# Performance work log

Measured on AMD Instinct MI355X. Metric: run time of the kernel, lower is better.

## Reference

```python
import jax, jax.numpy as jnp
import numpy as np

D = 1024
H = 16
N = 4096
D_K = D // H
SCALE = D_K ** 0.5


def setup_inputs() -> dict:
    key = jax.random.key(0)
    k_x, k_w = jax.random.split(key)
    X = jax.random.normal(k_x, (N, D), dtype=jnp.float32)
    # nn.Linear(D, 2*D, bias=False): weight [2D, D], y = X @ W.T
    Wqkv = jax.random.normal(k_w, (2 * D, D), dtype=jnp.float32) * (1.0 / np.sqrt(D))
    return {"X": X, "Wqkv": Wqkv}


def reference(X, Wqkv):
    n = X.shape[0]
    proj = X @ Wqkv.T                      # [N, 2D]
    qk, v = jnp.split(proj, 2, axis=-1)    # each [N, D]
    qk = qk.reshape(n, H, D_K)             # [N, H, d_k]
    v = v.reshape(n, H, D_K)
    s = jnp.einsum('nhd,mhd->hnm', qk, qk) / SCALE  # [H, N, N]
    a = jax.nn.softmax(s, axis=-1)
    ctx = jnp.einsum('hnm,mhd->nhd', a, v).reshape(n, H * D_K)
    return ctx
```

## Files before the change

kernel.cpp:

```cpp
#include <hip/hip_runtime.h>
#include <hip/hip_bf16.h>

#define N_TOK   4096
#define D_MODEL 1024
#define H_HEADS 16
#define DK      64
#define KVB     64
#define QK_PRESCALE 0.42466092f


typedef float  f32x4   __attribute__((ext_vector_type(4)));
typedef float  f32x16  __attribute__((ext_vector_type(16)));
typedef short  bf16x8  __attribute__((ext_vector_type(8)));

__device__ __forceinline__ ushort f2bf(float f) {
  union { float f; unsigned u; } v; v.f = f;
  unsigned u = v.u;
  u += 0x7fffu + ((u >> 16) & 1u);
  return (ushort)(u >> 16);
}

__device__ __forceinline__ unsigned cvt_pk_bf16(float lo, float hi) {
  unsigned r;
  asm("v_cvt_pk_bf16_f32 %0, %1, %2" : "=v"(r) : "v"(lo), "v"(hi));
  return r;
}

__device__ __forceinline__ float exp2_raw(float x) {
  float r;
  asm("v_exp_f32 %0, %1" : "=v"(r) : "v"(x));
  return r;
}

__device__ __forceinline__ void gload_lds16(const void* gsrc, void* ldst) {
  __builtin_amdgcn_global_load_lds(
      (const __attribute__((address_space(1))) unsigned int*)gsrc,
      (__attribute__((address_space(3))) unsigned int*)ldst, 16, 0, 0);
}

__device__ __forceinline__ f32x16 mfma32(bf16x8 a, bf16x8 b, f32x16 c) {
  return __builtin_amdgcn_mfma_f32_32x32x16_bf16(a, b, c, 0, 0, 0);
}

__device__ __forceinline__ void swap32(unsigned &a, unsigned &b) {
  asm("v_permlane32_swap_b32 %0, %1" : "+v"(a), "+v"(b));
}

__global__ __launch_bounds__(256) void cvt_bf16_kernel(
    const float* __restrict__ X, const float* __restrict__ W,
    ushort* __restrict__ Xb, ushort* __restrict__ Wb) {
  const size_t i = (size_t)blockIdx.x * 256 + threadIdx.x;
  const float* s;
  ushort* d;
  size_t off;
  if (i < 524288) { s = X; d = Xb; off = i * 8; }
  else            { s = W; d = Wb; off = (i - 524288) * 8; }
  float4 a = *(const float4*)(s + off);
  float4 b = *(const float4*)(s + off + 4);
  ushort4 lo, hi;
  lo.x = f2bf(a.x); lo.y = f2bf(a.y); lo.z = f2bf(a.z); lo.w = f2bf(a.w);
  hi.x = f2bf(b.x); hi.y = f2bf(b.y); hi.z = f2bf(b.z); hi.w = f2bf(b.w);
  *(ushort4*)(d + off)     = lo;
  *(ushort4*)(d + off + 4) = hi;
}

__global__ __launch_bounds__(256) void qkv_gemm_kernel(
    const ushort* __restrict__ Xb, const ushort* __restrict__ Wb,
    ushort* __restrict__ Qb, ushort* __restrict__ Vt) {
  __shared__ ushort As[2][128][32];
  __shared__ ushort Bs[2][128][32];

  const int tid  = threadIdx.x;
  const int lane = tid & 63;
  const int g    = lane >> 4;
  const int lr   = lane & 15;
  const int wave = tid >> 6;
  const int wr   = (wave >> 1) * 64;
  const int wc   = (wave & 1) * 64;

  const int bid = blockIdx.x;
  const int x   = bid & 7;
  const int i   = bid >> 3;
  const int rb  = (x >> 1) * 8 + (i >> 3);
  const int cb  = (x & 1) * 8 + (i & 7);

  f32x4 acc[4][4] = {};

  const int r0 = tid >> 2;
  const int c0 = (tid & 3) * 8;
  const ushort* xsrc = Xb + (size_t)(rb * 128 + r0) * D_MODEL + c0;
  const ushort* wsrc = Wb + (size_t)(cb * 128 + r0) * D_MODEL + c0;

#define GST(BUF, K0)                                                         \
  {                                                                          \
    gload_lds16(xsrc + (K0), (ushort*)As[BUF] + tid * 8);                    \
    gload_lds16(xsrc + 64 * D_MODEL + (K0), (ushort*)As[BUF] + (tid + 256) * 8); \
    gload_lds16(wsrc + (K0), (ushort*)Bs[BUF] + tid * 8);                    \
    gload_lds16(wsrc + 64 * D_MODEL + (K0), (ushort*)Bs[BUF] + (tid + 256) * 8); \
  }

  GST(0, 0);
  __syncthreads();

  for (int k0 = 0; k0 < D_MODEL; k0 += 32) {
    const int buf = (k0 >> 5) & 1;
    if (k0 + 32 < D_MODEL) GST(buf ^ 1, k0 + 32);

    bf16x8 a[4], b[4];
#pragma unroll
    for (int m = 0; m < 4; ++m) a[m] = *(const bf16x8*)&As[buf][wr + m * 16 + lr][g * 8];
#pragma unroll
    for (int n = 0; n < 4; ++n) b[n] = *(const bf16x8*)&Bs[buf][wc + n * 16 + lr][g * 8];

#pragma unroll
    for (int m = 0; m < 4; ++m)
#pragma unroll
      for (int n = 0; n < 4; ++n)
        acc[m][n] = __builtin_amdgcn_mfma_f32_16x16x32_bf16(a[m], b[n], acc[m][n], 0, 0, 0);
    __syncthreads();
  }

  const int nrow0 = rb * 128 + wr;
  const int jcol0 = cb * 128 + wc;
  if (cb < 8) {
#pragma unroll
    for (int m = 0; m < 4; ++m) {
      const int nn = nrow0 + m * 16 + 4 * g;
#pragma unroll
      for (int n = 0; n < 4; ++n) {
        const int j = jcol0 + n * 16 + lr;
#pragma unroll
        for (int r = 0; r < 4; ++r)
          Qb[(size_t)(nn + r) * D_MODEL + j] = f2bf(acc[m][n][r] * QK_PRESCALE);
      }
    }
  } else {
#pragma unroll
    for (int m = 0; m < 4; ++m) {
      const int nn = nrow0 + m * 16 + 4 * g;
#pragma unroll
      for (int n = 0; n < 4; ++n) {
        const int c = jcol0 - D_MODEL + n * 16 + lr;
        uint2 pv = { cvt_pk_bf16(acc[m][n][0], acc[m][n][1]),
                     cvt_pk_bf16(acc[m][n][2], acc[m][n][3]) };
        *(uint2*)(Vt + (size_t)c * N_TOK + nn) = pv;
      }
    }
  }
}

__global__ __launch_bounds__(512, 4) void attn_kernel(
    const ushort* __restrict__ Qb, const ushort* __restrict__ Vg,
    float* __restrict__ Out) {
  __shared__ __align__(16) char smem[65536];

  const int tid  = threadIdx.x;
  const int lane = tid & 63;
  const int l31  = lane & 31;
  const int hi   = lane >> 5;
  const int wave = tid >> 6;
  const int quad = wave >> 2;
  const int wq   = wave & 3;
  const int qtid = tid & 255;

  const int bid = blockIdx.x;
  const int i   = bid >> 3;
  const int h   = (bid & 7) * 2 + (i >> 5);
  const int qbase = (i & 31) * 128 + wq * 32;
  const int kvlo  = quad * (N_TOK / 2);
  const int nit   = (N_TOK / 2) / KVB;

  ushort* KtP = (ushort*)(smem + quad * 32768);
  ushort* VtP = (ushort*)(smem + quad * 32768 + 16384);

  bf16x8 qf[4];
  const ushort* qrow = Qb + (size_t)(qbase + l31) * D_MODEL + h * DK;
#pragma unroll
  for (int ks = 0; ks < 4; ++ks)
    qf[ks] = *(const bf16x8*)(qrow + ks * 16 + hi * 8);

  float l_run = 0.f;
  const f32x16 zz = {};
  f32x16 ctx0 = {}, ctx1 = {};

  const int srow = qtid >> 3;
  const int scg  = (qtid & 7) ^ (srow & 7);
  const ushort* kst = Qb + (size_t)(kvlo + srow) * D_MODEL + h * DK + scg * 8;
  const ushort* vst = Vg + (size_t)(h * DK + srow) * N_TOK + kvlo + scg * 8;

#define STAGE_ADV(BUF)                                                        \
  {                                                                           \
    ushort* kd = KtP + (BUF) * 4096 + (size_t)qtid * 8;                       \
    ushort* vd = VtP + (BUF) * 4096 + (size_t)qtid * 8;                       \
    gload_lds16(kst, kd);                                                     \
    gload_lds16(kst + 32 * D_MODEL, kd + 2048);                               \
    gload_lds16(vst, vd);                                                     \
    gload_lds16(vst + 32 * N_TOK, vd + 2048);                                 \
    kst += (size_t)KVB * D_MODEL;                                             \
    vst += KVB;                                                               \
  }

#define ATTN_BODY(BUF)                                                        \
  {                                                                           \
    if (stages_left > 0) { STAGE_ADV(BUF ^ 1); --stages_left; }               \
    f32x16 st0 = zz, st1 = zz;                                                \
    __builtin_amdgcn_s_setprio(1);                                            \
    _Pragma("unroll")                                                         \
    for (int ks = 0; ks < 4; ++ks) {                                          \
      bf16x8 kf0 = *(const bf16x8*)(KtP + (BUF) * 4096 + l31 * 64 +           \
                                    (((((ks << 1) | hi)) ^ (l31 & 7)) << 3)); \
      bf16x8 kf1 = *(const bf16x8*)(KtP + (BUF) * 4096 + (32 + l31) * 64 +    \
                                    (((((ks << 1) | hi)) ^ (l31 & 7)) << 3)); \
      st0 = mfma32(kf0, qf[ks], st0);                                         \
      st1 = mfma32(kf1, qf[ks], st1);                                         \
    }                                                                         \
    __builtin_amdgcn_s_setprio(0);                                            \
    float rsb[4];                                                             \
    unsigned pk0[8], pk1[8];                                                  \
    _Pragma("unroll")                                                         \
    for (int b = 0; b < 4; ++b) {                                             \
      float a0 = exp2_raw(st0[4 * b + 0]);                                    \
      float a1 = exp2_raw(st0[4 * b + 1]);                                    \
      float a2 = exp2_raw(st0[4 * b + 2]);                                    \
      float a3 = exp2_raw(st0[4 * b + 3]);                                    \
      float c0 = exp2_raw(st1[4 * b + 0]);                                    \
      float c1 = exp2_raw(st1[4 * b + 1]);                                    \
      float c2 = exp2_raw(st1[4 * b + 2]);                                    \
      float c3 = exp2_raw(st1[4 * b + 3]);                                    \
      rsb[b] = ((a0 + a1) + (a2 + a3)) + ((c0 + c1) + (c2 + c3));             \
      pk0[2 * b]     = cvt_pk_bf16(a0, a1);                                   \
      pk0[2 * b + 1] = cvt_pk_bf16(a2, a3);                                   \
      pk1[2 * b]     = cvt_pk_bf16(c0, c1);                                   \
      pk1[2 * b + 1] = cvt_pk_bf16(c2, c3);                                   \
    }                                                                         \
    l_run += (rsb[0] + rsb[1]) + (rsb[2] + rsb[3]);                           \
    _Pragma("unroll")                                                         \
    for (int kt = 0; kt < 2; ++kt) {                                          \
      _Pragma("unroll")                                                       \
      for (int km = 0; km < 2; ++km) {                                        \
        unsigned u0 = kt ? pk1[4 * km + 0] : pk0[4 * km + 0];                 \
        unsigned u1 = kt ? pk1[4 * km + 1] : pk0[4 * km + 1];                 \
        unsigned u2 = kt ? pk1[4 * km + 2] : pk0[4 * km + 2];                 \
        unsigned u3 = kt ? pk1[4 * km + 3] : pk0[4 * km + 3];                 \
        swap32(u0, u2);                                                       \
        swap32(u1, u3);                                                       \
        union { unsigned u[4]; bf16x8 v; } pf;                                \
        pf.u[0] = u0; pf.u[1] = u1; pf.u[2] = u2; pf.u[3] = u3;               \
        const int ck = (kt << 2) | (km << 1) | hi;                            \
        bf16x8 vf0 = *(const bf16x8*)(VtP + (BUF) * 4096 + l31 * 64 +         \
                                      ((ck ^ (l31 & 7)) << 3));               \
        bf16x8 vf1 = *(const bf16x8*)(VtP + (BUF) * 4096 + (32 + l31) * 64 +  \
                                      ((ck ^ (l31 & 7)) << 3));               \
        __builtin_amdgcn_s_setprio(1);                                        \
        ctx0 = mfma32(vf0, pf.v, ctx0);                                       \
        ctx1 = mfma32(vf1, pf.v, ctx1);                                       \
        __builtin_amdgcn_s_setprio(0);                                        \
      }                                                                       \
    }                                                                         \
    __syncthreads();                                                          \
  }

  int stages_left = nit - 1;
  STAGE_ADV(0);
  __syncthreads();

  for (int it = 0; it < nit; it += 2) {
    ATTN_BODY(0);
    ATTN_BODY(1);
  }

  l_run += __shfl_xor(l_run, 32);

  float* exA = (float*)smem;
  float* exB = (float*)(smem + 16384);
  float* exL = (float*)(smem + 32768);
  if (quad == 1) {
#pragma unroll
    for (int r = 0; r < 16; ++r) exA[(r * 4 + wq) * 64 + lane] = ctx0[r];
  } else {
#pragma unroll
    for (int r = 0; r < 16; ++r) exB[(r * 4 + wq) * 64 + lane] = ctx1[r];
  }
  exL[(quad * 4 + wq) * 64 + lane] = l_run;
  __syncthreads();

  const float lT  = l_run + exL[((1 - quad) * 4 + wq) * 64 + lane];
  const float inv = 1.f / lT;
  float* orow = Out + (size_t)(qbase + l31) * D_MODEL + h * DK;
  if (quad == 0) {
#pragma unroll
    for (int r = 0; r < 16; ++r) {
      const float v = ctx0[r] + exA[(r * 4 + wq) * 64 + lane];
      const int d = (r & 3) + 8 * (r >> 2) + 4 * hi;
      orow[d] = v * inv;
    }
  } else {
#pragma unroll
    for (int r = 0; r < 16; ++r) {
      const float v = ctx1[r] + exB[(r * 4 + wq) * 64 + lane];
      const int d = (r & 3) + 8 * (r >> 2) + 4 * hi;
      orow[32 + d] = v * inv;
    }
  }
}

extern "C" void kernel_launch(void* const* d_in, const int* in_sizes, int n_in,
                              void* d_out, int out_size, void* d_ws, size_t ws_size,
                              hipStream_t stream) {
  const float* X = (const float*)d_in[0];
  const float* W = (const float*)d_in[1];
  float* Out = (float*)d_out;

  ushort* Qb = (ushort*)d_ws;
  ushort* Vt = Qb + (size_t)N_TOK * D_MODEL;
  ushort* Xb = Vt + (size_t)N_TOK * D_MODEL;
  ushort* Wb = Xb + (size_t)N_TOK * D_MODEL;

  cvt_bf16_kernel<<<dim3(3072), dim3(256), 0, stream>>>(X, W, Xb, Wb);

  qkv_gemm_kernel<<<dim3(512), dim3(256), 0, stream>>>(Xb, Wb, Qb, Vt);

  attn_kernel<<<dim3(512), dim3(512), 0, stream>>>(Qb, Vt, Out);
}
```

Measured before the change: 124.8 us.

## Double attention block to 1024 threads covering 256 queries per head

The attention kernel now runs 16 waves per block: two groups of 8 waves each handle 256 query rows, and each group covers half of the key range. Each staged K/V tile in LDS is shared by 8 waves instead of 4, which halves the per-thread global-to-LDS loads and halves the grid to 256 blocks. The cross-group reduction of partial sums and context is rewritten to fit the 64KB LDS budget, at the cost of an extra barrier. The risks are that 256 blocks may underfill the GPU and that the larger blocks may lower occupancy.

After: 121.6 us. 1.03x faster.

```diff
diff --git a/kernel.cpp b/kernel.cpp
--- a/kernel.cpp
+++ b/kernel.cpp
@@ -149,29 +149,29 @@
   }
 }
 
-__global__ __launch_bounds__(512, 4) void attn_kernel(
+__global__ __launch_bounds__(1024, 4) void attn_kernel(
     const ushort* __restrict__ Qb, const ushort* __restrict__ Vg,
     float* __restrict__ Out) {
   __shared__ __align__(16) char smem[65536];
 
-  const int tid  = threadIdx.x;
-  const int lane = tid & 63;
-  const int l31  = lane & 31;
-  const int hi   = lane >> 5;
-  const int wave = tid >> 6;
-  const int quad = wave >> 2;
-  const int wq   = wave & 3;
-  const int qtid = tid & 255;
+  const int tid   = threadIdx.x;
+  const int lane  = tid & 63;
+  const int l31   = lane & 31;
+  const int hi    = lane >> 5;
+  const int wave  = tid >> 6;
+  const int octet = wave >> 3;
+  const int wq    = wave & 7;
+  const int otid  = tid & 511;
 
   const int bid = blockIdx.x;
   const int i   = bid >> 3;
-  const int h   = (bid & 7) * 2 + (i >> 5);
-  const int qbase = (i & 31) * 128 + wq * 32;
-  const int kvlo  = quad * (N_TOK / 2);
+  const int h   = (bid & 7) * 2 + (i >> 4);
+  const int qbase = (i & 15) * 256 + wq * 32;
+  const int kvlo  = octet * (N_TOK / 2);
   const int nit   = (N_TOK / 2) / KVB;
 
-  ushort* KtP = (ushort*)(smem + quad * 32768);
-  ushort* VtP = (ushort*)(smem + quad * 32768 + 16384);
+  ushort* KtP = (ushort*)(smem + octet * 32768);
+  ushort* VtP = KtP + 8192;
 
   bf16x8 qf[4];
   const ushort* qrow = Qb + (size_t)(qbase + l31) * D_MODEL + h * DK;
@@ -183,19 +183,15 @@
   const f32x16 zz = {};
   f32x16 ctx0 = {}, ctx1 = {};
 
-  const int srow = qtid >> 3;
-  const int scg  = (qtid & 7) ^ (srow & 7);
+  const int srow = otid >> 3;
+  const int scg  = (otid & 7) ^ (srow & 7);
   const ushort* kst = Qb + (size_t)(kvlo + srow) * D_MODEL + h * DK + scg * 8;
   const ushort* vst = Vg + (size_t)(h * DK + srow) * N_TOK + kvlo + scg * 8;
 
 #define STAGE_ADV(BUF)                                                        \
   {                                                                           \
-    ushort* kd = KtP + (BUF) * 4096 + (size_t)qtid * 8;                       \
-    ushort* vd = VtP + (BUF) * 4096 + (size_t)qtid * 8;                       \
-    gload_lds16(kst, kd);                                                     \
-    gload_lds16(kst + 32 * D_MODEL, kd + 2048);                               \
-    gload_lds16(vst, vd);                                                     \
-    gload_lds16(vst + 32 * N_TOK, vd + 2048);                                 \
+    gload_lds16(kst, KtP + (BUF) * 4096 + (size_t)otid * 8);                  \
+    gload_lds16(vst, VtP + (BUF) * 4096 + (size_t)otid * 8);                  \
     kst += (size_t)KVB * D_MODEL;                                             \
     vst += KVB;                                                               \
   }
@@ -271,33 +267,36 @@
 
   l_run += __shfl_xor(l_run, 32);
 
+  float* exL = (float*)smem;
+  exL[(octet * 8 + wq) * 64 + lane] = l_run;
+  __syncthreads();
+  const float lT  = exL[wq * 64 + lane] + exL[(8 + wq) * 64 + lane];
+  const float inv = 1.f / lT;
+  __syncthreads();
+
   float* exA = (float*)smem;
-  float* exB = (float*)(smem + 16384);
-  float* exL = (float*)(smem + 32768);
-  if (quad == 1) {
-#pragma unroll
-    for (int r = 0; r < 16; ++r) exA[(r * 4 + wq) * 64 + lane] = ctx0[r];
+  float* exB = (float*)(smem + 32768);
+  if (octet == 1) {
+#pragma unroll
+    for (int r = 0; r < 16; ++r) exA[(wq * 16 + r) * 64 + lane] = ctx0[r];
   } else {
 #pragma unroll
-    for (int r = 0; r < 16; ++r) exB[(r * 4 + wq) * 64 + lane] = ctx1[r];
-  }
-  exL[(quad * 4 + wq) * 64 + lane] = l_run;
-  __syncthreads();
-
-  const float lT  = l_run + exL[((1 - quad) * 4 + wq) * 64 + lane];
-  const float inv = 1.f / lT;
+    for (int r = 0; r < 16; ++r) exB[(wq * 16 + r) * 64 + lane] = ctx1[r];
+  }
+  __syncthreads();
+
   float* orow = Out + (size_t)(qbase + l31) * D_MODEL + h * DK;
-  if (quad == 0) {
+  if (octet == 0) {
 #pragma unroll
     for (int r = 0; r < 16; ++r) {
-      const float v = ctx0[r] + exA[(r * 4 + wq) * 64 + lane];
+      const float v = ctx0[r] + exA[(wq * 16 + r) * 64 + lane];
       const int d = (r & 3) + 8 * (r >> 2) + 4 * hi;
       orow[d] = v * inv;
     }
   } else {
 #pragma unroll
     for (int r = 0; r < 16; ++r) {
-      const float v = ctx1[r] + exB[(r * 4 + wq) * 64 + lane];
+      const float v = ctx1[r] + exB[(wq * 16 + r) * 64 + lane];
       const int d = (r & 3) + 8 * (r >> 2) + 4 * hi;
       orow[32 + d] = v * inv;
     }
@@ -320,5 +319,5 @@
 
   qkv_gemm_kernel<<<dim3(512), dim3(256), 0, stream>>>(Xb, Wb, Qb, Vt);
 
-  attn_kernel<<<dim3(512), dim3(512), 0, stream>>>(Qb, Vt, Out);
-}
+  attn_kernel<<<dim3(256), dim3(1024), 0, stream>>>(Qb, Vt, Out);
+}
```
